# Performance work log

Measured on AMD Instinct MI355X. Metric: run time of the kernel, lower is better.

## Reference

```python
import jax, jax.numpy as jnp
import numpy as np

N = 50000
DEG = 16
E = N * DEG
IN_F, HID, OUT_F = 512, 128, 64
SLOPE = 0.2


def setup_inputs() -> dict:
    key = jax.random.key(0)
    ks = jax.random.split(key, 10)
    row_ptr = jnp.arange(N + 1, dtype=jnp.int64) * DEG          # uniform-degree CSR
    col_idx = jax.random.randint(ks[0], (E,), 0, N, dtype=jnp.int64)
    x = jax.random.normal(ks[1], (N, IN_F), dtype=jnp.float32)
    s1 = 1.0 / np.sqrt(IN_F)
    s2 = 1.0 / np.sqrt(HID)
    return {
        "row_ptr": row_ptr,
        "col_idx": col_idx,
        "input_feature": x,
        "W1": jax.random.normal(ks[2], (IN_F, HID), dtype=jnp.float32) * s1,
        "attn_l1": jax.random.normal(ks[3], (HID,), dtype=jnp.float32) * s2,
        "attn_r1": jax.random.normal(ks[4], (HID,), dtype=jnp.float32) * s2,
        "bias1": jnp.zeros((HID,), dtype=jnp.float32),
        "W2": jax.random.normal(ks[5], (HID, OUT_F), dtype=jnp.float32) * s2,
        "attn_l2": jax.random.normal(ks[6], (OUT_F,), dtype=jnp.float32) * 0.125,
        "attn_r2": jax.random.normal(ks[7], (OUT_F,), dtype=jnp.float32) * 0.125,
        "bias2": jnp.zeros((OUT_F,), dtype=jnp.float32),
    }


def gat_layer(row_ptr, col_idx, x, W, attn_l, attn_r, bias):
    n = row_ptr.shape[0] - 1
    e = col_idx.shape[0]
    h = x @ W                                   # [N, F] dense GEMM
    el = h @ attn_l                             # [N] dst attention term
    er = h @ attn_r                             # [N] src attention term
    # edge -> destination row via CSR row_ptr
    dst = jnp.searchsorted(row_ptr, jnp.arange(e, dtype=row_ptr.dtype), side="right") - 1
    src = col_idx
    score = jax.nn.leaky_relu(el[dst] + er[src], negative_slope=SLOPE)  # [E]
    # neighborhood softmax over edges sharing a destination
    smax = jax.ops.segment_max(score, dst, num_segments=n)
    ex = jnp.exp(score - smax[dst])
    ssum = jax.ops.segment_sum(ex, dst, num_segments=n)
    alpha = ex / ssum[dst]                      # [E]
    # weighted gather-scatter aggregation
    out = jax.ops.segment_sum(alpha[:, None] * h[src], dst, num_segments=n)
    return out + bias


def reference(row_ptr, col_idx, input_feature, W1, attn_l1, attn_r1, bias1,
              W2, attn_l2, attn_r2, bias2):
    x = gat_layer(row_ptr, col_idx, input_feature, W1, attn_l1, attn_r1, bias1)
    x = gat_layer(row_ptr, col_idx, x, W2, attn_l2, attn_r2, bias2)
    return x
```

## Files before the change

### kernel.cpp

```cpp
#include <hip/hip_runtime.h>
#include <hip/hip_bf16.h>

#define Nn 50000
#define DEG 16
#define IN_F 512
#define HID 128
#define OUT_F 64
#define SLOPE 0.2f

typedef __attribute__((ext_vector_type(8))) short bf16x8;
typedef __attribute__((ext_vector_type(4))) float f32x4;
typedef __attribute__((ext_vector_type(4))) unsigned int u32x4;

__device__ __forceinline__ unsigned short f2bf(float f) {
    return __builtin_bit_cast(unsigned short, __float2bfloat16(f));
}
__device__ __forceinline__ float bf2f(unsigned short u) {
    return __bfloat162float(__builtin_bit_cast(__hip_bfloat16, u));
}

__global__ void __launch_bounds__(256) prep_kernel(
        const float* __restrict__ W1, const float* __restrict__ W2,
        const float* __restrict__ al1, const float* __restrict__ ar1,
        const float* __restrict__ b1, const int* __restrict__ row_ptr,
        unsigned short* __restrict__ w12t, float* __restrict__ uv,
        float* __restrict__ c2v, int* __restrict__ flag64) {
    const int tid = threadIdx.x;
    const int lane = tid & 63;
    const int w = tid >> 6;
    const int k = blockIdx.x * 4 + w;
    if (blockIdx.x == 0 && tid == 0) {
        *flag64 = (row_ptr[1] == DEG) ? 0 : 1;
    }
    const float* w1row = W1 + (size_t)k * HID;

    float acc = 0.f;
    #pragma unroll 8
    for (int j = 0; j < HID; ++j)
        acc += w1row[j] * W2[j * OUT_F + lane];
    w12t[(size_t)lane * IN_F + k] = f2bf(acc);

    float pu = w1row[lane] * al1[lane] + w1row[lane + 64] * al1[lane + 64];
    float pv = w1row[lane] * ar1[lane] + w1row[lane + 64] * ar1[lane + 64];
    #pragma unroll
    for (int m = 1; m < 64; m <<= 1) {
        pu += __shfl_xor(pu, m);
        pv += __shfl_xor(pv, m);
    }
    if (lane == 0) { uv[k] = pu; uv[IN_F + k] = pv; }

    if (blockIdx.x == 0 && w == 0) {
        float cacc = 0.f;
        #pragma unroll 8
        for (int j = 0; j < HID; ++j) cacc += b1[j] * W2[j * OUT_F + lane];
        c2v[lane] = cacc;
    }
}

template<int K>
__global__ void __launch_bounds__(256) gemm1_direct(
        const float* __restrict__ Af, const unsigned short* __restrict__ w12t,
        const float* __restrict__ uv,
        unsigned short* __restrict__ G, float* __restrict__ el,
        float* __restrict__ er, int M) {
    const int tid  = threadIdx.x;
    const int lane = tid & 63;
    const int w    = tid >> 6;
    const int ln   = lane & 15, q = lane >> 4;
    const int mb   = blockIdx.x * 64 + w * 16;

    int m0 = mb + ln; if (m0 > M - 1) m0 = M - 1;
    const float* a0p = Af + (size_t)m0 * K;

    f32x4 acc[4] = {};
    float sl = 0.f, sr = 0.f;

    #pragma unroll 4
    for (int ks = 0; ks < K / 32; ++ks) {
        const int kk = ks * 32 + q * 8;
        f32x4 ap0 = *(const f32x4*)(a0p + kk);
        f32x4 ap1 = *(const f32x4*)(a0p + kk + 4);
        f32x4 u0  = *(const f32x4*)(uv + kk);
        f32x4 u1_ = *(const f32x4*)(uv + kk + 4);
        f32x4 v0  = *(const f32x4*)(uv + K + kk);
        f32x4 v1_ = *(const f32x4*)(uv + K + kk + 4);
        bf16x8 af;
        #pragma unroll
        for (int jj = 0; jj < 4; ++jj) {
            af[jj]     = (short)f2bf(ap0[jj]);
            af[jj + 4] = (short)f2bf(ap1[jj]);
            sl += ap0[jj] * u0[jj] + ap1[jj] * u1_[jj];
            sr += ap0[jj] * v0[jj] + ap1[jj] * v1_[jj];
        }
        #pragma unroll
        for (int nt = 0; nt < 4; ++nt) {
            bf16x8 bfr = *(const bf16x8*)&w12t[(size_t)(nt * 16 + ln) * K + kk];
            acc[nt] = __builtin_amdgcn_mfma_f32_16x16x32_bf16(af, bfr, acc[nt], 0, 0, 0);
        }
    }

    sl += __shfl_xor(sl, 16); sl += __shfl_xor(sl, 32);
    sr += __shfl_xor(sr, 16); sr += __shfl_xor(sr, 32);
    if (q == 0 && mb + ln < M) { el[mb + ln] = sl; er[mb + ln] = sr; }

    #pragma unroll
    for (int r = 0; r < 4; ++r) {
        int grow = mb + q * 4 + r;
        if (grow < M) {
            #pragma unroll
            for (int nt = 0; nt < 4; ++nt)
                G[(size_t)grow * OUT_F + nt * 16 + ln] = f2bf(acc[nt][r]);
        }
    }
}

template<int MODE>
__global__ void __launch_bounds__(256) agg_k(
        const int* __restrict__ col, const int* __restrict__ flag64,
        const float* __restrict__ el, const float* __restrict__ er,
        const unsigned short* __restrict__ Hs, const float* __restrict__ addv,
        const float* __restrict__ alv, const float* __restrict__ arv,
        unsigned short* __restrict__ Ho, float* __restrict__ elo,
        float* __restrict__ ero, float* __restrict__ Fo) {
    const int tid  = threadIdx.x;
    const int lane = tid & 63;
    const int w    = tid >> 6;
    const int ln   = lane & 15, q = lane >> 4;
    const int node = blockIdx.x * 16 + w * 4 + q;
    const int use64 = *flag64;

    int e   = node * DEG + ln;
    int src = use64 ? (int)((const long long*)col)[e] : col[e];
    float sc = el[node] + er[src];
    sc = sc >= 0.f ? sc : SLOPE * sc;
    float mx = sc;
    #pragma unroll
    for (int m = 1; m < 16; m <<= 1) mx = fmaxf(mx, __shfl_xor(mx, m, 16));
    float ex = __expf(sc - mx);
    float sm = ex;
    #pragma unroll
    for (int m = 1; m < 16; m <<= 1) sm += __shfl_xor(sm, m, 16);
    float alpha = ex / sm;

    const int half = ln >> 3, cc = ln & 7;
    float a[8] = {};
    #pragma unroll
    for (int jj = 0; jj < DEG; jj += 2) {
        int   sj = __shfl(src, jj + half, 16);
        float aj = __shfl(alpha, jj + half, 16);
        bf16x8 hv = *(const bf16x8*)&Hs[(size_t)sj * OUT_F + cc * 8];
        #pragma unroll
        for (int c = 0; c < 8; ++c)
            a[c] += aj * bf2f((unsigned short)hv[c]);
    }
    #pragma unroll
    for (int c = 0; c < 8; ++c) {
        a[c] += __shfl_xor(a[c], 8, 16);
        a[c] += addv[cc * 8 + c];
    }

    if (MODE == 0) {
        float pl = 0.f, pr = 0.f;
        #pragma unroll
        for (int c = 0; c < 8; ++c) {
            pl += a[c] * alv[cc * 8 + c];
            pr += a[c] * arv[cc * 8 + c];
        }
        #pragma unroll
        for (int m = 1; m < 8; m <<= 1) {
            pl += __shfl_xor(pl, m, 16);
            pr += __shfl_xor(pr, m, 16);
        }
        if (ln == 0) { elo[node] = pl; ero[node] = pr; }
        if (half == 0) {
            unsigned int pk[4];
            #pragma unroll
            for (int c = 0; c < 4; ++c)
                pk[c] = (unsigned int)f2bf(a[2 * c]) |
                        ((unsigned int)f2bf(a[2 * c + 1]) << 16);
            *(u32x4*)&Ho[(size_t)node * OUT_F + cc * 8] = *(u32x4*)pk;
        }
    } else {
        if (half == 0) {
            f32x4 o0, o1;
            #pragma unroll
            for (int c = 0; c < 4; ++c) { o0[c] = a[c]; o1[c] = a[c + 4]; }
            *(f32x4*)&Fo[(size_t)node * OUT_F + cc * 8]     = o0;
            *(f32x4*)&Fo[(size_t)node * OUT_F + cc * 8 + 4] = o1;
        }
    }
}

extern "C" void kernel_launch(void* const* d_in, const int* in_sizes, int n_in,
                              void* d_out, int out_size, void* d_ws, size_t ws_size,
                              hipStream_t stream) {
    const int*   row_ptr = (const int*)d_in[0];
    const int*   col_idx = (const int*)d_in[1];
    const float* x   = (const float*)d_in[2];
    const float* W1  = (const float*)d_in[3];
    const float* al1 = (const float*)d_in[4];
    const float* ar1 = (const float*)d_in[5];
    const float* b1  = (const float*)d_in[6];
    const float* W2  = (const float*)d_in[7];
    const float* al2 = (const float*)d_in[8];
    const float* ar2 = (const float*)d_in[9];
    const float* b2  = (const float*)d_in[10];
    float* out = (float*)d_out;

    float* ws = (float*)d_ws;
    unsigned short* g   = (unsigned short*)ws;
    unsigned short* h2b = (unsigned short*)(ws + 1600000);
    float* el1 = ws + 3200000;
    float* er1 = ws + 3250000;
    float* el2 = ws + 3300000;
    float* er2 = ws + 3350000;
    unsigned short* w12t = (unsigned short*)(ws + 3400000);
    float* uv  = ws + 3420000;
    float* c2v = ws + 3421024;
    int* flag64 = (int*)(ws + 3421100);

    prep_kernel<<<128, 256, 0, stream>>>(
        W1, W2, al1, ar1, b1, row_ptr, w12t, uv, c2v, flag64);

    gemm1_direct<IN_F><<<(Nn + 63) / 64, 256, 0, stream>>>(
        x, w12t, uv, g, el1, er1, Nn);

    agg_k<0><<<Nn / 16, 256, 0, stream>>>(
        col_idx, flag64, el1, er1, g, c2v, al2, ar2, h2b, el2, er2, nullptr);

    agg_k<1><<<Nn / 16, 256, 0, stream>>>(
        col_idx, flag64, el2, er2, h2b, b2, nullptr, nullptr,
        nullptr, nullptr, nullptr, out);
}
```

Before: 241.9 us.

## Split GEMM1 K dimension across waves with shared-memory reduction

The first GEMM kernel now assigns each block 16 rows and splits the K=512 reduction across its 4 waves, each handling 128 columns. Each wave preloads all its A-tile loads up front, then partial MFMA accumulators and the attention dot products are reduced through LDS before writing G, el and er. This gives 4x more blocks and more independent loads in flight to better hide memory latency on the streaming read of x. In exchange it adds LDS traffic, a __syncthreads, and drops the M-boundary guard, which relies on N being divisible by 16.

```diff
diff --git a/kernel.cpp b/kernel.cpp
--- a/kernel.cpp
+++ b/kernel.cpp
@@ -58,59 +58,83 @@
 }
 
 template<int K>
-__global__ void __launch_bounds__(256) gemm1_direct(
+__global__ void __launch_bounds__(256) gemm1_splitk(
         const float* __restrict__ Af, const unsigned short* __restrict__ w12t,
         const float* __restrict__ uv,
         unsigned short* __restrict__ G, float* __restrict__ el,
         float* __restrict__ er, int M) {
+    constexpr int KW = K / 4;
+    constexpr int RS = 20;
+    __shared__ float red[4][64][RS];
+    __shared__ float redl[4][16];
+    __shared__ float redr[4][16];
+
     const int tid  = threadIdx.x;
     const int lane = tid & 63;
     const int w    = tid >> 6;
     const int ln   = lane & 15, q = lane >> 4;
-    const int mb   = blockIdx.x * 64 + w * 16;
+    const int mb   = blockIdx.x * 16;
 
     int m0 = mb + ln; if (m0 > M - 1) m0 = M - 1;
-    const float* a0p = Af + (size_t)m0 * K;
+    const float* a0p = Af + (size_t)m0 * K + w * KW + q * 8;
+    const float* up  = uv + w * KW + q * 8;
+    const float* vp  = uv + K + w * KW + q * 8;
+
+    f32x4 ap[4][2];
+    #pragma unroll
+    for (int ks = 0; ks < 4; ++ks) {
+        ap[ks][0] = *(const f32x4*)(a0p + ks * 32);
+        ap[ks][1] = *(const f32x4*)(a0p + ks * 32 + 4);
+    }
 
     f32x4 acc[4] = {};
     float sl = 0.f, sr = 0.f;
-
-    #pragma unroll 4
-    for (int ks = 0; ks < K / 32; ++ks) {
-        const int kk = ks * 32 + q * 8;
-        f32x4 ap0 = *(const f32x4*)(a0p + kk);
-        f32x4 ap1 = *(const f32x4*)(a0p + kk + 4);
-        f32x4 u0  = *(const f32x4*)(uv + kk);
-        f32x4 u1_ = *(const f32x4*)(uv + kk + 4);
-        f32x4 v0  = *(const f32x4*)(uv + K + kk);
-        f32x4 v1_ = *(const f32x4*)(uv + K + kk + 4);
+    #pragma unroll
+    for (int ks = 0; ks < 4; ++ks) {
+        f32x4 u0 = *(const f32x4*)(up + ks * 32);
+        f32x4 u1 = *(const f32x4*)(up + ks * 32 + 4);
+        f32x4 v0 = *(const f32x4*)(vp + ks * 32);
+        f32x4 v1 = *(const f32x4*)(vp + ks * 32 + 4);
         bf16x8 af;
         #pragma unroll
         for (int jj = 0; jj < 4; ++jj) {
-            af[jj]     = (short)f2bf(ap0[jj]);
-            af[jj + 4] = (short)f2bf(ap1[jj]);
-            sl += ap0[jj] * u0[jj] + ap1[jj] * u1_[jj];
-            sr += ap0[jj] * v0[jj] + ap1[jj] * v1_[jj];
+            af[jj]     = (short)f2bf(ap[ks][0][jj]);
+            af[jj + 4] = (short)f2bf(ap[ks][1][jj]);
+            sl += ap[ks][0][jj] * u0[jj] + ap[ks][1][jj] * u1[jj];
+            sr += ap[ks][0][jj] * v0[jj] + ap[ks][1][jj] * v1[jj];
         }
         #pragma unroll
         for (int nt = 0; nt < 4; ++nt) {
-            bf16x8 bfr = *(const bf16x8*)&w12t[(size_t)(nt * 16 + ln) * K + kk];
+            bf16x8 bfr = *(const bf16x8*)
+                &w12t[(size_t)(nt * 16 + ln) * K + w * KW + ks * 32 + q * 8];
             acc[nt] = __builtin_amdgcn_mfma_f32_16x16x32_bf16(af, bfr, acc[nt], 0, 0, 0);
         }
     }
+
+    #pragma unroll
+    for (int nt = 0; nt < 4; ++nt)
+        *(f32x4*)&red[w][nt * 16 + ln][q * 4] = acc[nt];
 
     sl += __shfl_xor(sl, 16); sl += __shfl_xor(sl, 32);
     sr += __shfl_xor(sr, 16); sr += __shfl_xor(sr, 32);
-    if (q == 0 && mb + ln < M) { el[mb + ln] = sl; er[mb + ln] = sr; }
-
-    #pragma unroll
-    for (int r = 0; r < 4; ++r) {
-        int grow = mb + q * 4 + r;
-        if (grow < M) {
-            #pragma unroll
-            for (int nt = 0; nt < 4; ++nt)
-                G[(size_t)grow * OUT_F + nt * 16 + ln] = f2bf(acc[nt][r]);
-        }
+    if (q == 0) { redl[w][ln] = sl; redr[w][ln] = sr; }
+    __syncthreads();
+
+    const int c  = tid & 63;
+    const int r0 = (tid >> 6) * 4;
+    f32x4 s = *(const f32x4*)&red[0][c][r0];
+    #pragma unroll
+    for (int ww = 1; ww < 4; ++ww) {
+        f32x4 p = *(const f32x4*)&red[ww][c][r0];
+        s += p;
+    }
+    #pragma unroll
+    for (int j = 0; j < 4; ++j)
+        G[(size_t)(mb + r0 + j) * OUT_F + c] = f2bf(s[j]);
+
+    if (tid < 16) {
+        el[mb + tid] = redl[0][tid] + redl[1][tid] + redl[2][tid] + redl[3][tid];
+        er[mb + tid] = redr[0][tid] + redr[1][tid] + redr[2][tid] + redr[3][tid];
     }
 }
 
@@ -222,7 +246,7 @@
     prep_kernel<<<128, 256, 0, stream>>>(
         W1, W2, al1, ar1, b1, row_ptr, w12t, uv, c2v, flag64);
 
-    gemm1_direct<IN_F><<<(Nn + 63) / 64, 256, 0, stream>>>(
+    gemm1_splitk<IN_F><<<Nn / 16, 256, 0, stream>>>(
         x, w12t, uv, g, el1, er1, Nn);
 
     agg_k<0><<<Nn / 16, 256, 0, stream>>>(
```

New measurement: 232.3 us. -3.9%, faster.
